# Kernel tuning notes

Hardware: AMD Instinct MI355X
Metric: run time of the kernel (lower is better)

Reference implementation:

```python
import jax, jax.numpy as jnp
import numpy as np

N = 50000
E = 800000
F_IN = 128
H = 64
C = 10
BN_EPS = 1e-5


def _glorot(key, shape):
    fan_in = shape[0]
    return jax.random.normal(key, shape, dtype=jnp.float32) / jnp.sqrt(jnp.float32(fan_in))


def setup_inputs() -> dict:
    key = jax.random.key(0)
    ks = jax.random.split(key, 16)
    inp = {
        "x": jax.random.normal(ks[0], (N, F_IN), dtype=jnp.float32),
        "edge_index": jax.random.randint(ks[1], (2, E), 0, N, dtype=jnp.int64),
    }
    # GINConv layer params: eps (train_eps=True, init 0), 2-layer MLP, BN affine
    dims = [(F_IN, H), (H, H), (H, H)]
    for i, (din, dout) in enumerate(dims, start=1):
        k1, k2 = jax.random.split(ks[1 + i], 2)
        inp[f"eps{i}"] = jnp.float32(0.0)
        inp[f"w{i}a"] = _glorot(k1, (din, H))
        inp[f"b{i}a"] = jnp.zeros((H,), jnp.float32)
        inp[f"w{i}b"] = _glorot(k2, (H, H))
        inp[f"b{i}b"] = jnp.zeros((H,), jnp.float32)
        inp[f"g{i}"] = jnp.ones((H,), jnp.float32)
        inp[f"be{i}"] = jnp.zeros((H,), jnp.float32)
    inp["lin_w"] = _glorot(ks[10], (H, C))
    inp["lin_b"] = jnp.zeros((C,), jnp.float32)
    return inp


def _gin_conv(x, src, dst, eps, wa, ba, wb, bb, g, be):
    # sum-aggregate neighbor features: scatter-add x[src] into dst rows
    agg = jax.ops.segment_sum(x[src], dst, num_segments=N)
    h = (1.0 + eps) * x + agg
    # MLP: Linear-ReLU-Linear-ReLU-BatchNorm1d (training-mode batch stats)
    h = jax.nn.relu(h @ wa + ba)
    h = jax.nn.relu(h @ wb + bb)
    mean = jnp.mean(h, axis=0)
    var = jnp.var(h, axis=0)
    return (h - mean) * jax.lax.rsqrt(var + BN_EPS) * g + be


def reference(x, edge_index,
              eps1, w1a, b1a, w1b, b1b, g1, be1,
              eps2, w2a, b2a, w2b, b2b, g2, be2,
              eps3, w3a, b3a, w3b, b3b, g3, be3,
              lin_w, lin_b):
    src, dst = edge_index[0], edge_index[1]
    h = jax.nn.relu(_gin_conv(x, src, dst, eps1, w1a, b1a, w1b, b1b, g1, be1))
    h = jax.nn.relu(_gin_conv(h, src, dst, eps2, w2a, b2a, w2b, b2b, g2, be2))
    h = jax.nn.relu(_gin_conv(h, src, dst, eps3, w3a, b3a, w3b, b3b, g3, be3))
    return h @ lin_w + lin_b
```

## Files before the change

### kernel.cpp

```cpp
#include <hip/hip_runtime.h>
#include <hip/hip_fp16.h>

#define NN 50000
#define NGROUP 3125
#define NCHUNK 391
#define CHCAP 3072
#define SLAB 8192
#define BN_EPS 1e-5f

typedef unsigned int uint;
typedef unsigned short ushort;
typedef _Float16 half8 __attribute__((ext_vector_type(8)));
typedef float floatx4 __attribute__((ext_vector_type(4)));

__device__ __forceinline__ int aswz(int slot) { return slot ^ ((slot >> 4) & 7); }

__device__ __forceinline__ float h_lo(uint u) {
    return __half2float(__ushort_as_half((ushort)(u & 0xFFFFu)));
}
__device__ __forceinline__ float h_hi(uint u) {
    return __half2float(__ushort_as_half((ushort)(u >> 16)));
}
__device__ __forceinline__ void unpack8(uint4 v, float* f) {
    f[0] = h_lo(v.x); f[1] = h_hi(v.x);
    f[2] = h_lo(v.y); f[3] = h_hi(v.y);
    f[4] = h_lo(v.z); f[5] = h_hi(v.z);
    f[6] = h_lo(v.w); f[7] = h_hi(v.w);
}

__global__ __launch_bounds__(256) void sortA_kernel(
    const int* __restrict__ ei, int* __restrict__ gcur,
    uint* __restrict__ bucket, int E)
{
    __shared__ int s_hist[NCHUNK];
    __shared__ int s_offs[NCHUNK];
    __shared__ int s_cur[NCHUNK];
    __shared__ int s_gb[NCHUNK];
    __shared__ int s_scanA[512], s_scanB[512];
    __shared__ uint s_sorted[SLAB];

    const int tid  = threadIdx.x;
    const int base = blockIdx.x * SLAB;
    const int cnt  = min(SLAB, E - base);

    for (int i = tid; i < NCHUNK; i += 256) s_hist[i] = 0;
    __syncthreads();

    uint pk[SLAB / 256];
    int nloc = 0;
    for (int i = tid; i < cnt; i += 256) {
        int src = ei[base + i];
        int dst = ei[E + base + i];
        int c = dst >> 7;
        pk[nloc++] = (uint)src | ((uint)(dst & 127) << 16) | ((uint)c << 23);
        atomicAdd(&s_hist[c], 1);
    }
    __syncthreads();
    for (int i = tid; i < 512; i += 256) s_scanA[i] = (i < NCHUNK) ? s_hist[i] : 0;
    __syncthreads();
    int* sa = s_scanA; int* sb = s_scanB;
    for (int off = 1; off < 512; off <<= 1) {
        for (int i = tid; i < 512; i += 256)
            sb[i] = sa[i] + ((i >= off) ? sa[i - off] : 0);
        __syncthreads();
        int* t = sa; sa = sb; sb = t;
    }
    for (int i = tid; i < NCHUNK; i += 256) {
        int excl = sa[i] - s_hist[i];
        s_offs[i] = excl;
        s_cur[i]  = excl;
    }
    __syncthreads();
    for (int k = 0; k < nloc; k++) {
        int c = pk[k] >> 23;
        int pos = atomicAdd(&s_cur[c], 1);
        s_sorted[pos] = pk[k];
    }
    __syncthreads();
    for (int c = tid; c < NCHUNK; c += 256) {
        int n = s_hist[c];
        s_gb[c] = n ? atomicAdd(&gcur[c], n) : 0;
    }
    __syncthreads();
    for (int i = tid; i < cnt; i += 256) {
        uint v = s_sorted[i];
        int c = v >> 23;
        int li = i - s_offs[c];
        bucket[(size_t)c * CHCAP + s_gb[c] + li] = v;
    }
}

__global__ __launch_bounds__(256) void fillB_kernel(
    const uint* __restrict__ bucket, const int* __restrict__ gcur,
    int* __restrict__ rowPtr, int* __restrict__ csr_src)
{
    __shared__ int s_hist[128];
    __shared__ int s_excl[128];
    __shared__ int s_cur[128];
    __shared__ int s_ws[4];
    __shared__ int s_base;
    const int c = blockIdx.x;
    const int tid = threadIdx.x;
    const int cnt = gcur[c];
    const int row0 = c * 128;

    int part = 0;
    for (int i = tid; i < c; i += 256) part += gcur[i];
    #pragma unroll
    for (int off = 32; off >= 1; off >>= 1) part += __shfl_down(part, off, 64);
    if ((tid & 63) == 0) s_ws[tid >> 6] = part;
    if (tid < 128) s_hist[tid] = 0;
    __syncthreads();
    if (tid == 0) s_base = s_ws[0] + s_ws[1] + s_ws[2] + s_ws[3];
    __syncthreads();
    const int base = s_base;
    if (tid == 0 && c == NCHUNK - 1) rowPtr[NN] = base + cnt;

    for (int i = tid; i < cnt; i += 256) {
        uint v = bucket[(size_t)c * CHCAP + i];
        atomicAdd(&s_hist[(v >> 16) & 127], 1);
    }
    __syncthreads();
    if (tid < 128) {
        int lane = tid & 63;
        int v = s_hist[tid];
        int incl = v;
        #pragma unroll
        for (int off = 1; off < 64; off <<= 1) {
            int t = __shfl_up(incl, off, 64);
            if (lane >= off) incl += t;
        }
        s_excl[tid] = incl - v;
    }
    __syncthreads();
    if (tid < 128) {
        int excl = s_excl[tid];
        if (tid >= 64) excl += s_excl[63] + s_hist[63];
        s_cur[tid] = excl;
        int row = row0 + tid;
        if (row < NN) rowPtr[row] = base + excl;
    }
    __syncthreads();
    for (int i = tid; i < cnt; i += 256) {
        uint v = bucket[(size_t)c * CHCAP + i];
        int dl  = (v >> 16) & 127;
        int src = v & 0xFFFFu;
        int ofs = atomicAdd(&s_cur[dl], 1);
        csr_src[base + ofs] = src;
    }
}

template<int FIN, bool APPLY>
__global__ __launch_bounds__(256, 4) void proj_kernel(
    const void* __restrict__ in_v,
    const float* __restrict__ stats_in, const float* __restrict__ g_in,
    const float* __restrict__ be_in,
    const float* __restrict__ wa,
    ushort* __restrict__ y_out)
{
    constexpr int KC = FIN / 32;
    __shared__ __align__(16) _Float16 s_B[FIN * 64];
    __shared__ __align__(16) _Float16 s_Y[4][1024];

    const int tid = threadIdx.x, w = tid >> 6, lane = tid & 63;
    const int q = lane >> 4, mm = lane & 15;

    for (int i = tid; i < FIN * 64; i += 256) {
        int j = i & 7, l = (i >> 3) & 63, t = i >> 9;
        int kc = t >> 2, nt = t & 3;
        int k = kc * 32 + (l >> 4) * 8 + j;
        int n = nt * 16 + (l & 15);
        s_B[i] = (_Float16)wa[k * 64 + n];
    }

    float scv[2][8], shv[2][8];
    if (APPLY) {
        #pragma unroll
        for (int kc = 0; kc < 2; kc++)
            #pragma unroll
            for (int j = 0; j < 8; j++) {
                int c = kc * 32 + q * 8 + j;
                float mean = stats_in[c] * (1.0f / NN);
                float var  = stats_in[64 + c] * (1.0f / NN) - mean * mean;
                float rstd = rsqrtf(var + BN_EPS);
                float s    = rstd * g_in[c];
                scv[kc][j] = s;
                shv[kc][j] = be_in[c] - mean * s;
            }
    }
    __syncthreads();

    int g = blockIdx.x * 4 + w;
    if (g >= NGROUP) return;
    const int row = g * 16 + mm;

    half8 af[KC];
    if (FIN == 128) {
        const float* xin = (const float*)in_v;
        #pragma unroll
        for (int kc = 0; kc < KC; kc++) {
            const float* p = xin + (size_t)row * 128 + kc * 32 + q * 8;
            float4 a = *(const float4*)p;
            float4 b = *(const float4*)(p + 4);
            half8 hv;
            hv[0] = (_Float16)a.x; hv[1] = (_Float16)a.y;
            hv[2] = (_Float16)a.z; hv[3] = (_Float16)a.w;
            hv[4] = (_Float16)b.x; hv[5] = (_Float16)b.y;
            hv[6] = (_Float16)b.z; hv[7] = (_Float16)b.w;
            af[kc] = hv;
        }
    } else {
        const ushort* hin = (const ushort*)in_v;
        #pragma unroll
        for (int kc = 0; kc < KC; kc++) {
            uint4 vv = *(const uint4*)(hin + (size_t)row * 64 + kc * 32 + q * 8);
            float f[8]; unpack8(vv, f);
            half8 hv;
            #pragma unroll
            for (int j = 0; j < 8; j++) {
                float z = APPLY ? fmaxf(fmaf(f[j], scv[kc][j], shv[kc][j]), 0.0f) : f[j];
                hv[j] = (_Float16)z;
            }
            af[kc] = hv;
        }
    }

    floatx4 acc[4] = {};
    #pragma unroll
    for (int nt = 0; nt < 4; nt++)
        #pragma unroll
        for (int kc = 0; kc < KC; kc++) {
            half8 bf = *(const half8*)(s_B + ((size_t)(kc * 4 + nt) * 64 + lane) * 8);
            acc[nt] = __builtin_amdgcn_mfma_f32_16x16x32_f16(af[kc], bf, acc[nt], 0, 0, 0);
        }

    _Float16* s_Yw = &s_Y[w][0];
    #pragma unroll
    for (int nt = 0; nt < 4; nt++)
        #pragma unroll
        for (int r = 0; r < 4; r++)
            s_Yw[(q * 4 + r) * 64 + nt * 16 + mm] = (_Float16)acc[nt][r];
    half8 t0 = *(const half8*)(s_Yw + lane * 8);
    half8 t1 = *(const half8*)(s_Yw + 512 + lane * 8);
    half8* dst = (half8*)((_Float16*)y_out + (size_t)g * 1024);
    dst[lane] = t0;
    dst[64 + lane] = t1;
}

__global__ __launch_bounds__(512, 4) void gin_gather_kernel(
    const ushort* __restrict__ y,
    const int* __restrict__ rowPtr, const int* __restrict__ csr_src,
    const float* __restrict__ eps_p, const float* __restrict__ ba,
    const float* __restrict__ wb, const float* __restrict__ bb,
    ushort* __restrict__ h_out, float* __restrict__ stats_out)
{
    __shared__ __align__(16) _Float16 s_B2[64 * 64];
    __shared__ __align__(16) _Float16 s_A[8][1024];
    __shared__ float s_red[8][64];

    const int tid = threadIdx.x, w = tid >> 6, lane = tid & 63;
    const int cc = lane & 7, gph = lane >> 3;
    const int q = lane >> 4, mm = lane & 15;

    for (int i = tid; i < 64 * 64; i += 512) {
        int j = i & 7, l = (i >> 3) & 63, t = i >> 9;
        int kc = t >> 2, nt = t & 3;
        int k = kc * 32 + (l >> 4) * 8 + j;
        int n = nt * 16 + (l & 15);
        s_B2[i] = (_Float16)wb[k * 64 + n];
    }

    const float eps1 = 1.0f + eps_p[0];
    float bav[8];
    #pragma unroll
    for (int j = 0; j < 8; j++) bav[j] = ba[8 * cc + j];
    float bbv[4];
    #pragma unroll
    for (int nt = 0; nt < 4; nt++) bbv[nt] = bb[nt * 16 + mm];
    __syncthreads();

    float bn_s[4] = {0.f, 0.f, 0.f, 0.f};
    float bn_q[4] = {0.f, 0.f, 0.f, 0.f};
    const uint4* y4 = (const uint4*)y;
    const int g = blockIdx.x * 8 + w;

    if (g < NGROUP) {
        const int row0 = g * 16;
        _Float16* s_Aw = &s_A[w][0];

        for (int m = 0; m < 16; m += 4) {
            int e[4], en[4], s[4];
            float a[4][8];
            uint4 v[4];
            #pragma unroll
            for (int i = 0; i < 4; i++) {
                int row = row0 + m + i;
                e[i] = rowPtr[row] + gph;
                en[i] = rowPtr[row + 1];
                #pragma unroll
                for (int j = 0; j < 8; j++) a[i][j] = 0.0f;
            }
            if (gph == 0) {
                #pragma unroll
                for (int i = 0; i < 4; i++) {
                    uint4 sv = y4[(size_t)(row0 + m + i) * 8 + cc];
                    float f[8]; unpack8(sv, f);
                    #pragma unroll
                    for (int j = 0; j < 8; j++) a[i][j] = eps1 * f[j];
                }
            }
            #pragma unroll
            for (int i = 0; i < 4; i++) s[i] = (e[i] < en[i]) ? csr_src[e[i]] : -1;
            #pragma unroll
            for (int i = 0; i < 4; i++) if (s[i] >= 0) v[i] = y4[(size_t)s[i] * 8 + cc];

            int mx = max(max(s[0], s[1]), max(s[2], s[3]));
            while (mx >= 0) {
                int n[4]; uint4 p[4];
                #pragma unroll
                for (int i = 0; i < 4; i++) {
                    n[i] = -1;
                    if (s[i] >= 0) { e[i] += 8; n[i] = (e[i] < en[i]) ? csr_src[e[i]] : -1; }
                }
                #pragma unroll
                for (int i = 0; i < 4; i++) if (n[i] >= 0) p[i] = y4[(size_t)n[i] * 8 + cc];
                #pragma unroll
                for (int i = 0; i < 4; i++) {
                    if (s[i] >= 0) {
                        float f[8]; unpack8(v[i], f);
                        #pragma unroll
                        for (int j = 0; j < 8; j++) a[i][j] += f[j];
                    }
                    s[i] = n[i]; v[i] = p[i];
                }
                mx = max(max(s[0], s[1]), max(s[2], s[3]));
            }

            #pragma unroll
            for (int off = 8; off < 64; off <<= 1)
                #pragma unroll
                for (int i = 0; i < 4; i++)
                    #pragma unroll
                    for (int j = 0; j < 8; j++)
                        a[i][j] += __shfl_xor(a[i][j], off, 64);

            if (gph == 0) {
                #pragma unroll
                for (int i = 0; i < 4; i++) {
                    half8 hv;
                    #pragma unroll
                    for (int j = 0; j < 8; j++)
                        hv[j] = (_Float16)fmaxf(a[i][j] + bav[j], 0.0f);
                    int slot = (cc >> 2) * 64 + (cc & 3) * 16 + (m + i);
                    *(half8*)(s_Aw + (size_t)aswz(slot) * 8) = hv;
                }
            }
        }

        half8 af2[2];
        #pragma unroll
        for (int kc = 0; kc < 2; kc++)
            af2[kc] = *(const half8*)(s_Aw + (size_t)aswz(kc * 64 + lane) * 8);
        floatx4 acc2[4] = {};
        #pragma unroll
        for (int nt = 0; nt < 4; nt++)
            #pragma unroll
            for (int kc = 0; kc < 2; kc++) {
                half8 bf = *(const half8*)(s_B2 + ((size_t)(kc * 4 + nt) * 64 + lane) * 8);
                acc2[nt] = __builtin_amdgcn_mfma_f32_16x16x32_f16(af2[kc], bf, acc2[nt], 0, 0, 0);
            }

        #pragma unroll
        for (int nt = 0; nt < 4; nt++)
            #pragma unroll
            for (int r = 0; r < 4; r++) {
                float val = fmaxf(acc2[nt][r] + bbv[nt], 0.0f);
                bn_s[nt] += val;
                bn_q[nt] += val * val;
                s_Aw[(q * 4 + r) * 64 + nt * 16 + mm] = (_Float16)val;
            }
        half8 t0 = *(const half8*)(s_Aw + lane * 8);
        half8 t1 = *(const half8*)(s_Aw + 512 + lane * 8);
        half8* dst = (half8*)((_Float16*)h_out + (size_t)row0 * 64);
        dst[lane] = t0;
        dst[64 + lane] = t1;
    }

    #pragma unroll
    for (int nt = 0; nt < 4; nt++) {
        bn_s[nt] += __shfl_xor(bn_s[nt], 16, 64);
        bn_s[nt] += __shfl_xor(bn_s[nt], 32, 64);
        bn_q[nt] += __shfl_xor(bn_q[nt], 16, 64);
        bn_q[nt] += __shfl_xor(bn_q[nt], 32, 64);
    }
    __syncthreads();
    if (lane < 16) {
        #pragma unroll
        for (int nt = 0; nt < 4; nt++) s_red[w][nt * 16 + lane] = bn_s[nt];
    }
    __syncthreads();
    if (w == 0) {
        float s = 0;
        #pragma unroll
        for (int j = 0; j < 8; j++) s += s_red[j][lane];
        atomicAdd(&stats_out[lane], s);
    }
    __syncthreads();
    if (lane < 16) {
        #pragma unroll
        for (int nt = 0; nt < 4; nt++) s_red[w][nt * 16 + lane] = bn_q[nt];
    }
    __syncthreads();
    if (w == 0) {
        float s = 0;
        #pragma unroll
        for (int j = 0; j < 8; j++) s += s_red[j][lane];
        atomicAdd(&stats_out[64 + lane], s);
    }
}

__global__ __launch_bounds__(256) void final_linear_kernel(
    const ushort* __restrict__ h, const float* __restrict__ stats,
    const float* __restrict__ g, const float* __restrict__ be,
    const float* __restrict__ w, const float* __restrict__ b,
    float* __restrict__ out)
{
    __shared__ float s_w[640];
    __shared__ float s_b[10];
    __shared__ float s_scale[64];
    __shared__ float s_shift[64];
    for (int i = threadIdx.x; i < 640; i += 256) s_w[i] = w[i];
    if (threadIdx.x < 10) s_b[threadIdx.x] = b[threadIdx.x];
    if (threadIdx.x < 64) {
        int c = threadIdx.x;
        float mean = stats[c] * (1.0f / NN);
        float var  = stats[64 + c] * (1.0f / NN) - mean * mean;
        float rstd = rsqrtf(var + BN_EPS);
        float s    = rstd * g[c];
        s_scale[c] = s;
        s_shift[c] = be[c] - mean * s;
    }
    __syncthreads();
    int row = blockIdx.x * 256 + threadIdx.x;
    if (row >= NN) return;
    float acc[10];
    #pragma unroll
    for (int c = 0; c < 10; c++) acc[c] = s_b[c];
    const uint4* hr = (const uint4*)(h + (size_t)row * 64);
    #pragma unroll
    for (int ch = 0; ch < 8; ch++) {
        uint4 v = hr[ch];
        float f[8]; unpack8(v, f);
        #pragma unroll
        for (int j = 0; j < 8; j++) {
            int k = ch * 8 + j;
            float val = fmaxf(fmaf(f[j], s_scale[k], s_shift[k]), 0.0f);
            #pragma unroll
            for (int c = 0; c < 10; c++) acc[c] = fmaf(val, s_w[k * 10 + c], acc[c]);
        }
    }
    #pragma unroll
    for (int c = 0; c < 10; c++) out[row * 10 + c] = acc[c];
}

extern "C" void kernel_launch(void* const* d_in, const int* in_sizes, int n_in,
                              void* d_out, int out_size, void* d_ws, size_t ws_size,
                              hipStream_t stream)
{
    const float* x  = (const float*)d_in[0];
    const int*   ei = (const int*)d_in[1];
    const int E = in_sizes[1] / 2;

    const float* eps[3]; const float* wa[3]; const float* ba[3];
    const float* wb[3];  const float* bb[3]; const float* g[3]; const float* be[3];
    for (int i = 0; i < 3; i++) {
        int base = 2 + 7 * i;
        eps[i] = (const float*)d_in[base + 0];
        wa[i]  = (const float*)d_in[base + 1];
        ba[i]  = (const float*)d_in[base + 2];
        wb[i]  = (const float*)d_in[base + 3];
        bb[i]  = (const float*)d_in[base + 4];
        g[i]   = (const float*)d_in[base + 5];
        be[i]  = (const float*)d_in[base + 6];
    }
    const float* lin_w = (const float*)d_in[23];
    const float* lin_b = (const float*)d_in[24];
    float* out = (float*)d_out;

    char*  base   = (char*)d_ws;
    int*   gcur   = (int*)base;
    float* stats  = (float*)(gcur + 512);
    int*   rowPtr = (int*)(stats + 384);
    uint*  bucket = (uint*)(rowPtr + NN + 1);
    int*   csrsrc = (int*)(bucket + (size_t)NCHUNK * CHCAP);
    size_t ioff   = (char*)(csrsrc + E) - base;
    ushort* yb    = (ushort*)(base + ((ioff + 15) & ~(size_t)15));
    ushort* hA    = yb + (size_t)NN * 64;
    ushort* hB    = hA + (size_t)NN * 64;

    hipMemsetAsync(gcur, 0, (512 + 384) * sizeof(int), stream);
    sortA_kernel<<<(E + SLAB - 1) / SLAB, 256, 0, stream>>>(ei, gcur, bucket, E);
    fillB_kernel<<<NCHUNK, 256, 0, stream>>>(bucket, gcur, rowPtr, csrsrc);

    const int PB = (NGROUP + 3) / 4;
    const int GB = (NGROUP + 7) / 8;

    proj_kernel<128, false><<<PB, 256, 0, stream>>>(
        x, nullptr, nullptr, nullptr, wa[0], yb);
    gin_gather_kernel<<<GB, 512, 0, stream>>>(
        yb, rowPtr, csrsrc, eps[0], ba[0], wb[0], bb[0], hA, stats);
    proj_kernel<64, true><<<PB, 256, 0, stream>>>(
        hA, stats, g[0], be[0], wa[1], yb);
    gin_gather_kernel<<<GB, 512, 0, stream>>>(
        yb, rowPtr, csrsrc, eps[1], ba[1], wb[1], bb[1], hB, stats + 128);
    proj_kernel<64, true><<<PB, 256, 0, stream>>>(
        hB, stats + 128, g[1], be[1], wa[2], yb);
    gin_gather_kernel<<<GB, 512, 0, stream>>>(
        yb, rowPtr, csrsrc, eps[2], ba[2], wb[2], bb[2], hA, stats + 256);
    final_linear_kernel<<<(NN + 255) / 256, 256, 0, stream>>>(
        hA, stats + 256, g[2], be[2], lin_w, lin_b, out);
}
```

Before: 299.3 us.

## Fuse edge bucketing with layer-1 projection and use packed half adds in gather

Merges the edge-sorting kernel and the first-layer projection into one launch, with blocks branching on their index and sharing a union of shared memory. This lets the independent projection work overlap with the sort and removes one launch. The sort now reads the edge list twice (a histogram pass, then a scatter pass) instead of keeping packed edges in registers. The gather kernel accumulates neighbour features with packed fp16 adds instead of unpacking to fp32, and shrinks blocks from 512 to 256 threads. The fp16 accumulation risks precision loss on high-degree nodes.

```diff
diff --git a/kernel.cpp b/kernel.cpp
--- a/kernel.cpp
+++ b/kernel.cpp
@@ -11,6 +11,7 @@
 typedef unsigned int uint;
 typedef unsigned short ushort;
 typedef _Float16 half8 __attribute__((ext_vector_type(8)));
+typedef _Float16 half2t __attribute__((ext_vector_type(2)));
 typedef float floatx4 __attribute__((ext_vector_type(4)));
 
 __device__ __forceinline__ int aswz(int slot) { return slot ^ ((slot >> 4) & 7); }
@@ -27,67 +28,133 @@
     f[4] = h_lo(v.z); f[5] = h_hi(v.z);
     f[6] = h_lo(v.w); f[7] = h_hi(v.w);
 }
-
-__global__ __launch_bounds__(256) void sortA_kernel(
+__device__ __forceinline__ uint pkadd(uint a, uint b) {
+    half2t x = __builtin_bit_cast(half2t, a);
+    half2t y = __builtin_bit_cast(half2t, b);
+    half2t r = x + y;
+    return __builtin_bit_cast(uint, r);
+}
+
+__global__ __launch_bounds__(256, 4) void sortA_proj1_kernel(
     const int* __restrict__ ei, int* __restrict__ gcur,
-    uint* __restrict__ bucket, int E)
+    uint* __restrict__ bucket, int E, int nsort,
+    const float* __restrict__ x, const float* __restrict__ wa,
+    ushort* __restrict__ y_out)
 {
-    __shared__ int s_hist[NCHUNK];
-    __shared__ int s_offs[NCHUNK];
-    __shared__ int s_cur[NCHUNK];
-    __shared__ int s_gb[NCHUNK];
-    __shared__ int s_scanA[512], s_scanB[512];
-    __shared__ uint s_sorted[SLAB];
-
-    const int tid  = threadIdx.x;
-    const int base = blockIdx.x * SLAB;
-    const int cnt  = min(SLAB, E - base);
-
-    for (int i = tid; i < NCHUNK; i += 256) s_hist[i] = 0;
-    __syncthreads();
-
-    uint pk[SLAB / 256];
-    int nloc = 0;
-    for (int i = tid; i < cnt; i += 256) {
-        int src = ei[base + i];
-        int dst = ei[E + base + i];
-        int c = dst >> 7;
-        pk[nloc++] = (uint)src | ((uint)(dst & 127) << 16) | ((uint)c << 23);
-        atomicAdd(&s_hist[c], 1);
-    }
-    __syncthreads();
-    for (int i = tid; i < 512; i += 256) s_scanA[i] = (i < NCHUNK) ? s_hist[i] : 0;
-    __syncthreads();
-    int* sa = s_scanA; int* sb = s_scanB;
-    for (int off = 1; off < 512; off <<= 1) {
-        for (int i = tid; i < 512; i += 256)
-            sb[i] = sa[i] + ((i >= off) ? sa[i - off] : 0);
+    __shared__ __align__(16) union {
+        struct {
+            int hist[NCHUNK]; int offs[NCHUNK]; int cur[NCHUNK]; int gb[NCHUNK];
+            int scanA[512]; int scanB[512];
+            uint sorted[SLAB];
+        } s;
+        struct {
+            _Float16 B[128 * 64];
+            _Float16 Y[4][1024];
+        } p;
+    } u;
+
+    const int tid = threadIdx.x;
+
+    if ((int)blockIdx.x < nsort) {
+        const int base = blockIdx.x * SLAB;
+        const int cnt  = min(SLAB, E - base);
+
+        for (int i = tid; i < NCHUNK; i += 256) u.s.hist[i] = 0;
         __syncthreads();
-        int* t = sa; sa = sb; sb = t;
-    }
-    for (int i = tid; i < NCHUNK; i += 256) {
-        int excl = sa[i] - s_hist[i];
-        s_offs[i] = excl;
-        s_cur[i]  = excl;
-    }
-    __syncthreads();
-    for (int k = 0; k < nloc; k++) {
-        int c = pk[k] >> 23;
-        int pos = atomicAdd(&s_cur[c], 1);
-        s_sorted[pos] = pk[k];
-    }
-    __syncthreads();
-    for (int c = tid; c < NCHUNK; c += 256) {
-        int n = s_hist[c];
-        s_gb[c] = n ? atomicAdd(&gcur[c], n) : 0;
-    }
-    __syncthreads();
-    for (int i = tid; i < cnt; i += 256) {
-        uint v = s_sorted[i];
-        int c = v >> 23;
-        int li = i - s_offs[c];
-        bucket[(size_t)c * CHCAP + s_gb[c] + li] = v;
-    }
+        for (int i = tid; i < cnt; i += 256) {
+            int dst = ei[E + base + i];
+            atomicAdd(&u.s.hist[dst >> 7], 1);
+        }
+        __syncthreads();
+        for (int i = tid; i < 512; i += 256) u.s.scanA[i] = (i < NCHUNK) ? u.s.hist[i] : 0;
+        __syncthreads();
+        int* sa = u.s.scanA; int* sb = u.s.scanB;
+        for (int off = 1; off < 512; off <<= 1) {
+            for (int i = tid; i < 512; i += 256)
+                sb[i] = sa[i] + ((i >= off) ? sa[i - off] : 0);
+            __syncthreads();
+            int* t = sa; sa = sb; sb = t;
+        }
+        for (int i = tid; i < NCHUNK; i += 256) {
+            int excl = sa[i] - u.s.hist[i];
+            u.s.offs[i] = excl;
+            u.s.cur[i]  = excl;
+        }
+        __syncthreads();
+        for (int i = tid; i < cnt; i += 256) {
+            int src = ei[base + i];
+            int dst = ei[E + base + i];
+            int c = dst >> 7;
+            uint v = (uint)src | ((uint)(dst & 127) << 16) | ((uint)c << 23);
+            int pos = atomicAdd(&u.s.cur[c], 1);
+            u.s.sorted[pos] = v;
+        }
+        __syncthreads();
+        for (int c = tid; c < NCHUNK; c += 256) {
+            int n = u.s.hist[c];
+            u.s.gb[c] = n ? atomicAdd(&gcur[c], n) : 0;
+        }
+        __syncthreads();
+        for (int i = tid; i < cnt; i += 256) {
+            uint v = u.s.sorted[i];
+            int c = v >> 23;
+            int li = i - u.s.offs[c];
+            bucket[(size_t)c * CHCAP + u.s.gb[c] + li] = v;
+        }
+        return;
+    }
+
+    const int w = tid >> 6, lane = tid & 63;
+    const int q = lane >> 4, mm = lane & 15;
+
+    _Float16* s_B = u.p.B;
+    for (int i = tid; i < 128 * 64; i += 256) {
+        int j = i & 7, l = (i >> 3) & 63, t = i >> 9;
+        int kc = t >> 2, nt = t & 3;
+        int k = kc * 32 + (l >> 4) * 8 + j;
+        int n = nt * 16 + (l & 15);
+        s_B[i] = (_Float16)wa[k * 64 + n];
+    }
+    __syncthreads();
+
+    int g = ((int)blockIdx.x - nsort) * 4 + w;
+    if (g >= NGROUP) return;
+    const int row = g * 16 + mm;
+
+    half8 af[4];
+    #pragma unroll
+    for (int kc = 0; kc < 4; kc++) {
+        const float* ptr = x + (size_t)row * 128 + kc * 32 + q * 8;
+        float4 a = *(const float4*)ptr;
+        float4 b = *(const float4*)(ptr + 4);
+        half8 hv;
+        hv[0] = (_Float16)a.x; hv[1] = (_Float16)a.y;
+        hv[2] = (_Float16)a.z; hv[3] = (_Float16)a.w;
+        hv[4] = (_Float16)b.x; hv[5] = (_Float16)b.y;
+        hv[6] = (_Float16)b.z; hv[7] = (_Float16)b.w;
+        af[kc] = hv;
+    }
+
+    floatx4 acc[4] = {};
+    #pragma unroll
+    for (int nt = 0; nt < 4; nt++)
+        #pragma unroll
+        for (int kc = 0; kc < 4; kc++) {
+            half8 bf = *(const half8*)(s_B + ((size_t)(kc * 4 + nt) * 64 + lane) * 8);
+            acc[nt] = __builtin_amdgcn_mfma_f32_16x16x32_f16(af[kc], bf, acc[nt], 0, 0, 0);
+        }
+
+    _Float16* s_Yw = &u.p.Y[w][0];
+    #pragma unroll
+    for (int nt = 0; nt < 4; nt++)
+        #pragma unroll
+        for (int r = 0; r < 4; r++)
+            s_Yw[(q * 4 + r) * 64 + nt * 16 + mm] = (_Float16)acc[nt][r];
+    half8 t0 = *(const half8*)(s_Yw + lane * 8);
+    half8 t1 = *(const half8*)(s_Yw + 512 + lane * 8);
+    half8* dst = (half8*)((_Float16*)y_out + (size_t)g * 1024);
+    dst[lane] = t0;
+    dst[64 + lane] = t1;
 }
 
 __global__ __launch_bounds__(256) void fillB_kernel(
@@ -247,7 +314,7 @@
     dst[64 + lane] = t1;
 }
 
-__global__ __launch_bounds__(512, 4) void gin_gather_kernel(
+__global__ __launch_bounds__(256, 4) void gin_gather_kernel(
     const ushort* __restrict__ y,
     const int* __restrict__ rowPtr, const int* __restrict__ csr_src,
     const float* __restrict__ eps_p, const float* __restrict__ ba,
@@ -255,14 +322,14 @@
     ushort* __restrict__ h_out, float* __restrict__ stats_out)
 {
     __shared__ __align__(16) _Float16 s_B2[64 * 64];
-    __shared__ __align__(16) _Float16 s_A[8][1024];
-    __shared__ float s_red[8][64];
+    __shared__ __align__(16) _Float16 s_A[4][1024];
+    __shared__ float s_red[4][64];
 
     const int tid = threadIdx.x, w = tid >> 6, lane = tid & 63;
     const int cc = lane & 7, gph = lane >> 3;
     const int q = lane >> 4, mm = lane & 15;
 
-    for (int i = tid; i < 64 * 64; i += 512) {
+    for (int i = tid; i < 64 * 64; i += 256) {
         int j = i & 7, l = (i >> 3) & 63, t = i >> 9;
         int kc = t >> 2, nt = t & 3;
         int k = kc * 32 + (l >> 4) * 8 + j;
@@ -282,7 +349,7 @@
     float bn_s[4] = {0.f, 0.f, 0.f, 0.f};
     float bn_q[4] = {0.f, 0.f, 0.f, 0.f};
     const uint4* y4 = (const uint4*)y;
-    const int g = blockIdx.x * 8 + w;
+    const int g = blockIdx.x * 4 + w;
 
     if (g < NGROUP) {
         const int row0 = g * 16;
@@ -290,24 +357,14 @@
 
         for (int m = 0; m < 16; m += 4) {
             int e[4], en[4], s[4];
-            float a[4][8];
             uint4 v[4];
+            uint4 pk[4];
             #pragma unroll
             for (int i = 0; i < 4; i++) {
                 int row = row0 + m + i;
                 e[i] = rowPtr[row] + gph;
                 en[i] = rowPtr[row + 1];
-                #pragma unroll
-                for (int j = 0; j < 8; j++) a[i][j] = 0.0f;
-            }
-            if (gph == 0) {
-                #pragma unroll
-                for (int i = 0; i < 4; i++) {
-                    uint4 sv = y4[(size_t)(row0 + m + i) * 8 + cc];
-                    float f[8]; unpack8(sv, f);
-                    #pragma unroll
-                    for (int j = 0; j < 8; j++) a[i][j] = eps1 * f[j];
-                }
+                pk[i].x = pk[i].y = pk[i].z = pk[i].w = 0u;
             }
             #pragma unroll
             for (int i = 0; i < 4; i++) s[i] = (e[i] < en[i]) ? csr_src[e[i]] : -1;
@@ -327,13 +384,27 @@
                 #pragma unroll
                 for (int i = 0; i < 4; i++) {
                     if (s[i] >= 0) {
-                        float f[8]; unpack8(v[i], f);
-                        #pragma unroll
-                        for (int j = 0; j < 8; j++) a[i][j] += f[j];
+                        pk[i].x = pkadd(pk[i].x, v[i].x);
+                        pk[i].y = pkadd(pk[i].y, v[i].y);
+                        pk[i].z = pkadd(pk[i].z, v[i].z);
+                        pk[i].w = pkadd(pk[i].w, v[i].w);
                     }
                     s[i] = n[i]; v[i] = p[i];
                 }
                 mx = max(max(s[0], s[1]), max(s[2], s[3]));
+            }
+
+            float a[4][8];
+            #pragma unroll
+            for (int i = 0; i < 4; i++) unpack8(pk[i], a[i]);
+            if (gph == 0) {
+                #pragma unroll
+                for (int i = 0; i < 4; i++) {
+                    uint4 sv = y4[(size_t)(row0 + m + i) * 8 + cc];
+                    float f[8]; unpack8(sv, f);
+                    #pragma unroll
+                    for (int j = 0; j < 8; j++) a[i][j] = fmaf(eps1, f[j], a[i][j]);
+                }
             }
 
             #pragma unroll
@@ -402,7 +473,7 @@
     if (w == 0) {
         float s = 0;
         #pragma unroll
-        for (int j = 0; j < 8; j++) s += s_red[j][lane];
+        for (int j = 0; j < 4; j++) s += s_red[j][lane];
         atomicAdd(&stats_out[lane], s);
     }
     __syncthreads();
@@ -414,7 +485,7 @@
     if (w == 0) {
         float s = 0;
         #pragma unroll
-        for (int j = 0; j < 8; j++) s += s_red[j][lane];
+        for (int j = 0; j < 4; j++) s += s_red[j][lane];
         atomicAdd(&stats_out[64 + lane], s);
     }
 }
@@ -498,24 +569,23 @@
     ushort* hA    = yb + (size_t)NN * 64;
     ushort* hB    = hA + (size_t)NN * 64;
 
+    const int SB = (E + SLAB - 1) / SLAB;
+    const int PB = (NGROUP + 3) / 4;
+    const int GB = (NGROUP + 3) / 4;
+
     hipMemsetAsync(gcur, 0, (512 + 384) * sizeof(int), stream);
-    sortA_kernel<<<(E + SLAB - 1) / SLAB, 256, 0, stream>>>(ei, gcur, bucket, E);
+    sortA_proj1_kernel<<<SB + PB, 256, 0, stream>>>(ei, gcur, bucket, E, SB, x, wa[0], yb);
     fillB_kernel<<<NCHUNK, 256, 0, stream>>>(bucket, gcur, rowPtr, csrsrc);
 
-    const int PB = (NGROUP + 3) / 4;
-    const int GB = (NGROUP + 7) / 8;
-
-    proj_kernel<128, false><<<PB, 256, 0, stream>>>(
-        x, nullptr, nullptr, nullptr, wa[0], yb);
-    gin_gather_kernel<<<GB, 512, 0, stream>>>(
+    gin_gather_kernel<<<GB, 256, 0, stream>>>(
         yb, rowPtr, csrsrc, eps[0], ba[0], wb[0], bb[0], hA, stats);
     proj_kernel<64, true><<<PB, 256, 0, stream>>>(
         hA, stats, g[0], be[0], wa[1], yb);
-    gin_gather_kernel<<<GB, 512, 0, stream>>>(
+    gin_gather_kernel<<<GB, 256, 0, stream>>>(
         yb, rowPtr, csrsrc, eps[1], ba[1], wb[1], bb[1], hB, stats + 128);
     proj_kernel<64, true><<<PB, 256, 0, stream>>>(
         hB, stats + 128, g[1], be[1], wa[2], yb);
-    gin_gather_kernel<<<GB, 512, 0, stream>>>(
+    gin_gather_kernel<<<GB, 256, 0, stream>>>(
         yb, rowPtr, csrsrc, eps[2], ba[2], wb[2], bb[2], hA, stats + 256);
     final_linear_kernel<<<(NN + 255) / 256, 256, 0, stream>>>(
         hA, stats + 256, g[2], be[2], lin_w, lin_b, out);
```

After: 336.7 us. 12.5% more time.

## Split gather rows across warps, accumulate in packed fp16, shrink sort slab

Applied to the files above, without the earlier changes.

The gather kernel now gives each of the four warps per 16-row group four rows, instead of one warp looping over all sixteen rows. It accumulates neighbour sums with packed half2 adds rather than converting each value to fp32, and only one warp per group runs the second MFMA and the batch-norm stats. The sort kernel uses smaller slabs, re-reads edges in a second pass instead of holding them in registers, and gets higher occupancy bounds. The fp16 accumulation can lose precision on high-degree nodes, and the extra block sync plus idle warps during the MFMA stage may offset the added parallelism.

```diff
diff --git a/kernel.cpp b/kernel.cpp
--- a/kernel.cpp
+++ b/kernel.cpp
@@ -5,12 +5,13 @@
 #define NGROUP 3125
 #define NCHUNK 391
 #define CHCAP 3072
-#define SLAB 8192
+#define SLAB 2048
 #define BN_EPS 1e-5f
 
 typedef unsigned int uint;
 typedef unsigned short ushort;
 typedef _Float16 half8 __attribute__((ext_vector_type(8)));
+typedef _Float16 half2t __attribute__((ext_vector_type(2)));
 typedef float floatx4 __attribute__((ext_vector_type(4)));
 
 __device__ __forceinline__ int aswz(int slot) { return slot ^ ((slot >> 4) & 7); }
@@ -27,8 +28,14 @@
     f[4] = h_lo(v.z); f[5] = h_hi(v.z);
     f[6] = h_lo(v.w); f[7] = h_hi(v.w);
 }
-
-__global__ __launch_bounds__(256) void sortA_kernel(
+__device__ __forceinline__ uint pkadd(uint a, uint b) {
+    half2t x = __builtin_bit_cast(half2t, a);
+    half2t y = __builtin_bit_cast(half2t, b);
+    half2t r = x + y;
+    return __builtin_bit_cast(uint, r);
+}
+
+__global__ __launch_bounds__(256, 4) void sortA_kernel(
     const int* __restrict__ ei, int* __restrict__ gcur,
     uint* __restrict__ bucket, int E)
 {
@@ -45,15 +52,9 @@
 
     for (int i = tid; i < NCHUNK; i += 256) s_hist[i] = 0;
     __syncthreads();
-
-    uint pk[SLAB / 256];
-    int nloc = 0;
     for (int i = tid; i < cnt; i += 256) {
-        int src = ei[base + i];
         int dst = ei[E + base + i];
-        int c = dst >> 7;
-        pk[nloc++] = (uint)src | ((uint)(dst & 127) << 16) | ((uint)c << 23);
-        atomicAdd(&s_hist[c], 1);
+        atomicAdd(&s_hist[dst >> 7], 1);
     }
     __syncthreads();
     for (int i = tid; i < 512; i += 256) s_scanA[i] = (i < NCHUNK) ? s_hist[i] : 0;
@@ -71,10 +72,13 @@
         s_cur[i]  = excl;
     }
     __syncthreads();
-    for (int k = 0; k < nloc; k++) {
-        int c = pk[k] >> 23;
+    for (int i = tid; i < cnt; i += 256) {
+        int src = ei[base + i];
+        int dst = ei[E + base + i];
+        int c = dst >> 7;
+        uint v = (uint)src | ((uint)(dst & 127) << 16) | ((uint)c << 23);
         int pos = atomicAdd(&s_cur[c], 1);
-        s_sorted[pos] = pk[k];
+        s_sorted[pos] = v;
     }
     __syncthreads();
     for (int c = tid; c < NCHUNK; c += 256) {
@@ -247,7 +251,7 @@
     dst[64 + lane] = t1;
 }
 
-__global__ __launch_bounds__(512, 4) void gin_gather_kernel(
+__global__ __launch_bounds__(512, 8) void gin_gather_kernel(
     const ushort* __restrict__ y,
     const int* __restrict__ rowPtr, const int* __restrict__ csr_src,
     const float* __restrict__ eps_p, const float* __restrict__ ba,
@@ -255,10 +259,12 @@
     ushort* __restrict__ h_out, float* __restrict__ stats_out)
 {
     __shared__ __align__(16) _Float16 s_B2[64 * 64];
-    __shared__ __align__(16) _Float16 s_A[8][1024];
-    __shared__ float s_red[8][64];
+    __shared__ __align__(16) _Float16 s_A[2][1024];
+    __shared__ float s_red[2][128];
 
     const int tid = threadIdx.x, w = tid >> 6, lane = tid & 63;
+    const int gl = w >> 2;
+    const int m  = (w & 3) * 4;
     const int cc = lane & 7, gph = lane >> 3;
     const int q = lane >> 4, mm = lane & 15;
 
@@ -269,93 +275,100 @@
         int n = nt * 16 + (l & 15);
         s_B2[i] = (_Float16)wb[k * 64 + n];
     }
+    if (tid < 256) ((float*)s_red)[tid] = 0.0f;
 
     const float eps1 = 1.0f + eps_p[0];
     float bav[8];
     #pragma unroll
     for (int j = 0; j < 8; j++) bav[j] = ba[8 * cc + j];
-    float bbv[4];
-    #pragma unroll
-    for (int nt = 0; nt < 4; nt++) bbv[nt] = bb[nt * 16 + mm];
-    __syncthreads();
-
-    float bn_s[4] = {0.f, 0.f, 0.f, 0.f};
-    float bn_q[4] = {0.f, 0.f, 0.f, 0.f};
+    __syncthreads();
+
     const uint4* y4 = (const uint4*)y;
-    const int g = blockIdx.x * 8 + w;
+    const int g = blockIdx.x * 2 + gl;
 
     if (g < NGROUP) {
         const int row0 = g * 16;
-        _Float16* s_Aw = &s_A[w][0];
-
-        for (int m = 0; m < 16; m += 4) {
-            int e[4], en[4], s[4];
-            float a[4][8];
-            uint4 v[4];
+        _Float16* s_Aw = &s_A[gl][0];
+
+        int e[4], en[4], s[4];
+        uint4 v[4];
+        uint4 pk[4];
+        #pragma unroll
+        for (int i = 0; i < 4; i++) {
+            int row = row0 + m + i;
+            e[i] = rowPtr[row] + gph;
+            en[i] = rowPtr[row + 1];
+            pk[i].x = pk[i].y = pk[i].z = pk[i].w = 0u;
+        }
+        #pragma unroll
+        for (int i = 0; i < 4; i++) s[i] = (e[i] < en[i]) ? csr_src[e[i]] : -1;
+        #pragma unroll
+        for (int i = 0; i < 4; i++) if (s[i] >= 0) v[i] = y4[(size_t)s[i] * 8 + cc];
+
+        int mx = max(max(s[0], s[1]), max(s[2], s[3]));
+        while (mx >= 0) {
+            int n[4]; uint4 p[4];
             #pragma unroll
             for (int i = 0; i < 4; i++) {
-                int row = row0 + m + i;
-                e[i] = rowPtr[row] + gph;
-                en[i] = rowPtr[row + 1];
+                n[i] = -1;
+                if (s[i] >= 0) { e[i] += 8; n[i] = (e[i] < en[i]) ? csr_src[e[i]] : -1; }
+            }
+            #pragma unroll
+            for (int i = 0; i < 4; i++) if (n[i] >= 0) p[i] = y4[(size_t)n[i] * 8 + cc];
+            #pragma unroll
+            for (int i = 0; i < 4; i++) {
+                if (s[i] >= 0) {
+                    pk[i].x = pkadd(pk[i].x, v[i].x);
+                    pk[i].y = pkadd(pk[i].y, v[i].y);
+                    pk[i].z = pkadd(pk[i].z, v[i].z);
+                    pk[i].w = pkadd(pk[i].w, v[i].w);
+                }
+                s[i] = n[i]; v[i] = p[i];
+            }
+            mx = max(max(s[0], s[1]), max(s[2], s[3]));
+        }
+
+        float a[4][8];
+        #pragma unroll
+        for (int i = 0; i < 4; i++) unpack8(pk[i], a[i]);
+        if (gph == 0) {
+            #pragma unroll
+            for (int i = 0; i < 4; i++) {
+                uint4 sv = y4[(size_t)(row0 + m + i) * 8 + cc];
+                float f[8]; unpack8(sv, f);
                 #pragma unroll
-                for (int j = 0; j < 8; j++) a[i][j] = 0.0f;
-            }
-            if (gph == 0) {
+                for (int j = 0; j < 8; j++) a[i][j] = fmaf(eps1, f[j], a[i][j]);
+            }
+        }
+
+        #pragma unroll
+        for (int off = 8; off < 64; off <<= 1)
+            #pragma unroll
+            for (int i = 0; i < 4; i++)
                 #pragma unroll
-                for (int i = 0; i < 4; i++) {
-                    uint4 sv = y4[(size_t)(row0 + m + i) * 8 + cc];
-                    float f[8]; unpack8(sv, f);
-                    #pragma unroll
-                    for (int j = 0; j < 8; j++) a[i][j] = eps1 * f[j];
-                }
-            }
-            #pragma unroll
-            for (int i = 0; i < 4; i++) s[i] = (e[i] < en[i]) ? csr_src[e[i]] : -1;
-            #pragma unroll
-            for (int i = 0; i < 4; i++) if (s[i] >= 0) v[i] = y4[(size_t)s[i] * 8 + cc];
-
-            int mx = max(max(s[0], s[1]), max(s[2], s[3]));
-            while (mx >= 0) {
-                int n[4]; uint4 p[4];
+                for (int j = 0; j < 8; j++)
+                    a[i][j] += __shfl_xor(a[i][j], off, 64);
+
+        if (gph == 0) {
+            #pragma unroll
+            for (int i = 0; i < 4; i++) {
+                half8 hv;
                 #pragma unroll
-                for (int i = 0; i < 4; i++) {
-                    n[i] = -1;
-                    if (s[i] >= 0) { e[i] += 8; n[i] = (e[i] < en[i]) ? csr_src[e[i]] : -1; }
-                }
-                #pragma unroll
-                for (int i = 0; i < 4; i++) if (n[i] >= 0) p[i] = y4[(size_t)n[i] * 8 + cc];
-                #pragma unroll
-                for (int i = 0; i < 4; i++) {
-                    if (s[i] >= 0) {
-                        float f[8]; unpack8(v[i], f);
-                        #pragma unroll
-                        for (int j = 0; j < 8; j++) a[i][j] += f[j];
-                    }
-                    s[i] = n[i]; v[i] = p[i];
-                }
-                mx = max(max(s[0], s[1]), max(s[2], s[3]));
-            }
-
-            #pragma unroll
-            for (int off = 8; off < 64; off <<= 1)
-                #pragma unroll
-                for (int i = 0; i < 4; i++)
-                    #pragma unroll
-                    for (int j = 0; j < 8; j++)
-                        a[i][j] += __shfl_xor(a[i][j], off, 64);
-
-            if (gph == 0) {
-                #pragma unroll
-                for (int i = 0; i < 4; i++) {
-                    half8 hv;
-                    #pragma unroll
-                    for (int j = 0; j < 8; j++)
-                        hv[j] = (_Float16)fmaxf(a[i][j] + bav[j], 0.0f);
-                    int slot = (cc >> 2) * 64 + (cc & 3) * 16 + (m + i);
-                    *(half8*)(s_Aw + (size_t)aswz(slot) * 8) = hv;
-                }
-            }
-        }
+                for (int j = 0; j < 8; j++)
+                    hv[j] = (_Float16)fmaxf(a[i][j] + bav[j], 0.0f);
+                int slot = (cc >> 2) * 64 + (cc & 3) * 16 + (m + i);
+                *(half8*)(s_Aw + (size_t)aswz(slot) * 8) = hv;
+            }
+        }
+    }
+    __syncthreads();
+
+    if ((w & 3) == 0 && g < NGROUP) {
+        const int row0 = g * 16;
+        _Float16* s_Aw = &s_A[gl][0];
+        float bbv[4];
+        #pragma unroll
+        for (int nt = 0; nt < 4; nt++) bbv[nt] = bb[nt * 16 + mm];
 
         half8 af2[2];
         #pragma unroll
@@ -370,6 +383,8 @@
                 acc2[nt] = __builtin_amdgcn_mfma_f32_16x16x32_f16(af2[kc], bf, acc2[nt], 0, 0, 0);
             }
 
+        float bn_s[4] = {0.f, 0.f, 0.f, 0.f};
+        float bn_q[4] = {0.f, 0.f, 0.f, 0.f};
         #pragma unroll
         for (int nt = 0; nt < 4; nt++)
             #pragma unroll
@@ -384,38 +399,26 @@
         half8* dst = (half8*)((_Float16*)h_out + (size_t)row0 * 64);
         dst[lane] = t0;
         dst[64 + lane] = t1;
-    }
-
-    #pragma unroll
-    for (int nt = 0; nt < 4; nt++) {
-        bn_s[nt] += __shfl_xor(bn_s[nt], 16, 64);
-        bn_s[nt] += __shfl_xor(bn_s[nt], 32, 64);
-        bn_q[nt] += __shfl_xor(bn_q[nt], 16, 64);
-        bn_q[nt] += __shfl_xor(bn_q[nt], 32, 64);
-    }
-    __syncthreads();
-    if (lane < 16) {
-        #pragma unroll
-        for (int nt = 0; nt < 4; nt++) s_red[w][nt * 16 + lane] = bn_s[nt];
+
+        #pragma unroll
+        for (int nt = 0; nt < 4; nt++) {
+            bn_s[nt] += __shfl_xor(bn_s[nt], 16, 64);
+            bn_s[nt] += __shfl_xor(bn_s[nt], 32, 64);
+            bn_q[nt] += __shfl_xor(bn_q[nt], 16, 64);
+            bn_q[nt] += __shfl_xor(bn_q[nt], 32, 64);
+        }
+        if (lane < 16) {
+            #pragma unroll
+            for (int nt = 0; nt < 4; nt++) {
+                s_red[gl][nt * 16 + lane]      = bn_s[nt];
+                s_red[gl][64 + nt * 16 + lane] = bn_q[nt];
+            }
+        }
     }
     __syncthreads();
     if (w == 0) {
-        float s = 0;
-        #pragma unroll
-        for (int j = 0; j < 8; j++) s += s_red[j][lane];
-        atomicAdd(&stats_out[lane], s);
-    }
-    __syncthreads();
-    if (lane < 16) {
-        #pragma unroll
-        for (int nt = 0; nt < 4; nt++) s_red[w][nt * 16 + lane] = bn_q[nt];
-    }
-    __syncthreads();
-    if (w == 0) {
-        float s = 0;
-        #pragma unroll
-        for (int j = 0; j < 8; j++) s += s_red[j][lane];
-        atomicAdd(&stats_out[64 + lane], s);
+        atomicAdd(&stats_out[lane],      s_red[0][lane]      + s_red[1][lane]);
+        atomicAdd(&stats_out[64 + lane], s_red[0][64 + lane] + s_red[1][64 + lane]);
     }
 }
 
@@ -498,12 +501,13 @@
     ushort* hA    = yb + (size_t)NN * 64;
     ushort* hB    = hA + (size_t)NN * 64;
 
+    const int SB = (E + SLAB - 1) / SLAB;
+    const int PB = (NGROUP + 3) / 4;
+    const int GB = (NGROUP + 1) / 2;
+
     hipMemsetAsync(gcur, 0, (512 + 384) * sizeof(int), stream);
-    sortA_kernel<<<(E + SLAB - 1) / SLAB, 256, 0, stream>>>(ei, gcur, bucket, E);
+    sortA_kernel<<<SB, 256, 0, stream>>>(ei, gcur, bucket, E);
     fillB_kernel<<<NCHUNK, 256, 0, stream>>>(bucket, gcur, rowPtr, csrsrc);
-
-    const int PB = (NGROUP + 3) / 4;
-    const int GB = (NGROUP + 7) / 8;
 
     proj_kernel<128, false><<<PB, 256, 0, stream>>>(
         x, nullptr, nullptr, nullptr, wa[0], yb);
```

After: 405.0 us. 35.3% more time.
